# Performance work log

Measured on AMD Instinct MI355X. Metric: run time of the kernel, lower is better.

Reference implementation:

```python
import jax, jax.numpy as jnp
import numpy as np
import math

BLOCK = 4      # block_size
N_HEADS = 8
DIM = 512
COND = 512
B = 2
HWU = 32       # h = w = u
NN = 7         # 'cross' neighbors


def _layernorm(x, w, eps=1e-5):
    mu = x.mean(-1, keepdims=True)
    var = ((x - mu) ** 2).mean(-1, keepdims=True)
    return (x - mu) * jax.lax.rsqrt(var + eps) * w


def _modulate(x, shift, scale):
    return x * (1.0 + scale) + shift


def _rotate_half(x):
    x1, x2 = jnp.split(x, 2, axis=-1)
    return jnp.concatenate([-x2, x1], axis=-1)


def _rot(x, cos, sin):
    return x * cos + _rotate_half(x) * sin


def setup_inputs() -> dict:
    key = jax.random.key(0)
    ks = jax.random.split(key, 16)
    h = w = u = HWU
    S = h * w * u
    dh = DIM // N_HEADS
    P = BLOCK ** 3
    ib = HWU // BLOCK                       # blocks per axis = 8
    nb = ib ** 3                            # 512 blocks per batch

    x = jax.random.normal(ks[0], (B, S, DIM), jnp.float32)
    c = jax.random.normal(ks[1], (B, COND), jnp.float32)

    # proper rotary tables over P block-local positions
    inv = 1.0 / (10000.0 ** (np.arange(0, dh, 2, dtype=np.float32) / dh))
    f = np.arange(P, dtype=np.float32)[:, None] * inv[None, :]
    emb = np.concatenate([f, f], axis=-1)          # [P, dh]
    cos = jnp.asarray(np.cos(emb))[None, :, None, :]
    sin = jnp.asarray(np.sin(emb))[None, :, None, :]

    # neighbor indices (cross pattern) on the block grid, mirroring get_neighbor_indices
    grid = np.stack(np.meshgrid(np.arange(B), np.arange(ib), np.arange(ib), np.arange(ib), indexing='ij'), axis=-1)
    shifts = np.array([[0, 0, 0, 0], [0, 0, -1, 0], [0, -1, 0, 0], [0, 0, 0, -1],
                       [0, 0, 1, 0], [0, 1, 0, 0], [0, 0, 0, 1]])
    nbr = grid[..., None, :] + shifts[None, None, None, None, :, :]
    nbr[..., 1:] = np.clip(nbr[..., 1:], 0, ib - 1)
    flat = (nbr[..., 0] * ib * ib * ib + nbr[..., 1] * ib * ib
            + nbr[..., 2] * ib + nbr[..., 3]).reshape(B * nb, NN)
    # every other block is 'nonzero' -> Nsel = 512
    nonzero_blocks = np.arange(0, B * nb, 2, dtype=np.int64)
    nonzero_blocks_neighbor = flat[nonzero_blocks].reshape(-1).astype(np.int64)

    s = 0.02
    params = dict(
        norm1_w=jnp.ones((DIM,), jnp.float32),
        qkv_w=s * jax.random.normal(ks[2], (3 * DIM, DIM), jnp.float32),
        out_w=s * jax.random.normal(ks[3], (DIM, DIM), jnp.float32),
        norm2_w=jnp.ones((DIM,), jnp.float32),
        mlp_w1=s * jax.random.normal(ks[4], (4 * DIM, DIM), jnp.float32),
        mlp_b1=jnp.zeros((4 * DIM,), jnp.float32),
        mlp_w2=s * jax.random.normal(ks[5], (DIM, 4 * DIM), jnp.float32),
        mlp_b2=jnp.zeros((DIM,), jnp.float32),
        adaln_w=s * jax.random.normal(ks[6], (6 * DIM, COND), jnp.float32),
        adaln_b=jnp.zeros((6 * DIM,), jnp.float32),
        kv_empty=s * jax.random.normal(ks[7], (1, P, 2 * DIM), jnp.float32),
    )
    return dict(x=x, c=c, cos_q=cos, sin_q=sin, cos_k=cos, sin_k=sin,
                nonzero_blocks=jnp.asarray(nonzero_blocks),
                nonzero_blocks_neighbor=jnp.asarray(nonzero_blocks_neighbor),
                h=h, w=w, u=u, **params)


def reference(x, c, cos_q, sin_q, cos_k, sin_k, nonzero_blocks, nonzero_blocks_neighbor,
              h, w, u, norm1_w, qkv_w, out_w, norm2_w, mlp_w1, mlp_b1, mlp_w2, mlp_b2,
              adaln_w, adaln_b, kv_empty):
    Bx, S, D = x.shape
    bs = BLOCK
    ix, iy, iz = h // bs, w // bs, u // bs
    nb = ix * iy * iz
    P = bs ** 3
    dh = D // N_HEADS
    Nsel = nonzero_blocks.shape[0]

    def transform(t):
        t = t.reshape(Bx, ix, bs, iy, bs, iz, bs, D)
        return t.transpose(0, 1, 3, 5, 2, 4, 6, 7).reshape(Bx, nb, P, D)

    def inverse_transform(t):
        t = t.reshape(Bx, ix, iy, iz, bs, bs, bs, D)
        return t.transpose(0, 1, 4, 2, 5, 3, 6, 7).reshape(Bx, S, D)

    mods = (c @ adaln_w.T + adaln_b)[:, None, :]         # [B,1,6D]
    shift_msa, scale_msa, gate_msa, shift_mlp, scale_mlp, gate_mlp = jnp.split(mods, 6, axis=-1)

    x_skip = x
    xm = _modulate(_layernorm(x, norm1_w), shift_msa, scale_msa)
    xb = transform(xm).reshape(Bx * nb, P, D)
    x_sel = xb[nonzero_blocks]                            # [Nsel,P,D]

    qkv = x_sel @ qkv_w.T                                 # [Nsel,P,3D]
    q, k, v = jnp.split(qkv, 3, axis=-1)
    k_e, v_e = jnp.split(kv_empty, 2, axis=-1)            # [1,P,D]
    k_full = jnp.broadcast_to(k_e, (Bx * nb, P, D)).at[nonzero_blocks].set(k)
    v_full = jnp.broadcast_to(v_e, (Bx * nb, P, D)).at[nonzero_blocks].set(v)
    kn = k_full[nonzero_blocks_neighbor]                  # [Nsel*NN,P,D]
    vn = v_full[nonzero_blocks_neighbor]

    qh = _rot(q.reshape(Nsel, P, N_HEADS, dh), cos_q, sin_q)
    kh = _rot(kn.reshape(Nsel * NN, P, N_HEADS, dh), cos_k, sin_k)
    kh = kh.reshape(Nsel, NN * P, N_HEADS, dh)
    vh = vn.reshape(Nsel, NN * P, N_HEADS, dh)

    scores = jnp.einsum('bqhd,bkhd->bhqk', qh, kh) / math.sqrt(dh)
    attn = jax.nn.softmax(scores, axis=-1)
    out = jnp.einsum('bhqk,bkhd->bqhd', attn, vh).reshape(Nsel, P, D)

    xz = jnp.zeros((Bx * nb, P, D), out.dtype).at[nonzero_blocks].set(out)
    x_attn = inverse_transform(xz.reshape(Bx, nb, P, D))
    x1 = x_skip + gate_msa * (x_attn @ out_w.T)

    x2 = _modulate(_layernorm(x1, norm2_w), shift_mlp, scale_mlp)
    mlp = jax.nn.gelu(x2 @ mlp_w1.T + mlp_b1, approximate=True) @ mlp_w2.T + mlp_b2
    return x1 + gate_mlp * mlp
```

## Files before the change

kernel.cpp:

```cpp
#include <hip/hip_runtime.h>
#include <cstdint>
#include <cstddef>

typedef unsigned short u16;
typedef __attribute__((ext_vector_type(8))) __bf16 bf16x8;
typedef __attribute__((ext_vector_type(4))) float f32x4;

typedef __attribute__((address_space(1))) const void GAS;
typedef __attribute__((address_space(3))) void LAS;

__device__ __forceinline__ void gld_lds16(const void* g, void* l) {
  __builtin_amdgcn_global_load_lds((GAS*)g, (LAS*)l, 16, 0, 0);
}

__device__ __forceinline__ u16 f2bf(float f) {
  union { float f; unsigned u; } x; x.f = f;
  unsigned r = x.u + 0x7FFFu + ((x.u >> 16) & 1u);
  return (u16)(r >> 16);
}
__device__ __forceinline__ float bf2f(u16 s) {
  union { unsigned u; float f; } x; x.u = ((unsigned)s) << 16;
  return x.f;
}
__device__ __forceinline__ f32x4 mfma16(bf16x8 a, bf16x8 b, f32x4 c) {
  return __builtin_amdgcn_mfma_f32_16x16x32_bf16(a, b, c, 0, 0, 0);
}


__global__ void selmap_k(const int* __restrict__ nzb, int* __restrict__ map) {
  int t = threadIdx.x;
  map[t] = -1;
  __syncthreads();
  if (t < 512) map[nzb[t]] = t;
}

__global__ __launch_bounds__(256) void castw_k(const float* __restrict__ in,
                                               u16* __restrict__ out, int n4) {
  int i = blockIdx.x * 256 + threadIdx.x;
  if (i >= n4) return;
  float4 v = ((const float4*)in)[i];
  u16 o[4] = {f2bf(v.x), f2bf(v.y), f2bf(v.z), f2bf(v.w)};
  ((uint2*)out)[i] = *(uint2*)o;
}

__global__ __launch_bounds__(256) void adaln_k(const float* __restrict__ c,
    const float* __restrict__ w, const float* __restrict__ b, float* __restrict__ mods) {
  int j = blockIdx.x * 256 + threadIdx.x;
  int bt = blockIdx.y;
  const float4* cr = (const float4*)(c + bt * 512);
  const float4* wr = (const float4*)(w + (size_t)j * 512);
  float s = 0.f;
  #pragma unroll 4
  for (int k = 0; k < 128; ++k) {
    float4 a = wr[k], q = cr[k];
    s += a.x * q.x + a.y * q.y + a.z * q.z + a.w * q.w;
  }
  mods[bt * 3072 + j] = s + b[j];
}

__global__ __launch_bounds__(256) void kvempty_k(const float* __restrict__ kve,
    const float* __restrict__ cT, const float* __restrict__ sT,
    u16* __restrict__ kempty, u16* __restrict__ vTempty) {
  int T = blockIdx.x * 256 + threadIdx.x;
  int h = T >> 12, p = (T >> 6) & 63, d = T & 63;
  float kv = kve[p * 1024 + h * 64 + d];
  float pv = kve[p * 1024 + h * 64 + (d ^ 32)];
  float cs = cT[p * 64 + d], sn = sT[p * 64 + d];
  float r = kv * cs + ((d < 32) ? -pv : pv) * sn;
  kempty[(h * 64 + p) * 64 + d] = f2bf(r);
  vTempty[(h * 64 + d) * 64 + p] = f2bf(kve[p * 1024 + 512 + h * 64 + d]);
}


__global__ __launch_bounds__(256) void ln1_k(const float* __restrict__ x,
    const float* __restrict__ nw, const float* __restrict__ mods,
    const int* __restrict__ nzb, u16* __restrict__ xm) {
  int row = blockIdx.x * 4 + (threadIdx.x >> 6);
  int t = threadIdx.x & 63;
  int sel = row >> 6, p = row & 63;
  int g = nzb[sel];
  int bt = g >> 9, blk = g & 511;
  int s = (blk >> 6) * 4096 + (p >> 4) * 1024 + ((blk >> 3) & 7) * 128
        + ((p >> 2) & 3) * 32 + (blk & 7) * 4 + (p & 3);
  const float* src = x + ((size_t)bt * 32768 + s) * 512;
  int d0 = t * 8;
  float4 a = *(const float4*)(src + d0);
  float4 b = *(const float4*)(src + d0 + 4);
  float v[8] = {a.x, a.y, a.z, a.w, b.x, b.y, b.z, b.w};
  float sum = 0.f, sq = 0.f;
  #pragma unroll
  for (int j = 0; j < 8; ++j) { sum += v[j]; sq += v[j] * v[j]; }
  #pragma unroll
  for (int m = 1; m < 64; m <<= 1) {
    sum += __shfl_xor(sum, m, 64);
    sq  += __shfl_xor(sq, m, 64);
  }
  float mean = sum * (1.f / 512.f);
  float var = sq * (1.f / 512.f) - mean * mean;
  float rstd = rsqrtf(var + 1e-5f);
  const float* mb = mods + bt * 3072;
  u16 o[8];
  #pragma unroll
  for (int j = 0; j < 8; ++j) {
    int d = d0 + j;
    float xn = (v[j] - mean) * rstd * nw[d];
    o[j] = f2bf(xn * (1.f + mb[512 + d]) + mb[d]);
  }
  *(uint4*)(xm + (size_t)row * 512 + d0) = *(uint4*)o;
}


template <int EPI>
__global__ __launch_bounds__(512, 2) void gemm256(const u16* __restrict__ A,
    const u16* __restrict__ W, int M, int N, int K, void* __restrict__ outp,
    const float* __restrict__ bias, const u16* __restrict__ x1,
    const float* __restrict__ mods, int rowOff, int NB) {
  __shared__ u16 L[65536];
  const int nwg = gridDim.x;
  const int cpx = nwg >> 3;
  const int tile = ((int)blockIdx.x & 7) * cpx + ((int)blockIdx.x >> 3);
  const int bm = (tile / NB) * 256, bn = (tile % NB) * 256;
  const int tid = threadIdx.x;
  const int w = tid >> 6, l = tid & 63, lr = l & 15, lg = l >> 4;
  const int wr = w >> 2, wc = w & 3;

  const u16* ga[4];
  const u16* gb[4];
  #pragma unroll
  for (int i = 0; i < 4; ++i) {
    int s = i * 512 + tid;
    int r = s >> 3, c = (s & 7) ^ (r & 7);
    ga[i] = A + (size_t)(bm + r) * K + c * 8;
    gb[i] = W + (size_t)(bn + r) * K + c * 8;
  }

  f32x4 acc[8][4];
  #pragma unroll
  for (int i = 0; i < 8; ++i)
    #pragma unroll
    for (int j = 0; j < 4; ++j) acc[i][j] = (f32x4){0.f, 0.f, 0.f, 0.f};

  auto STAGE = [&](int kt, int buf) {
    u16* lb = L + buf * 32768;
    #pragma unroll
    for (int i = 0; i < 4; ++i) {
      gld_lds16(ga[i] + (size_t)kt * 64, lb + (i * 512 + tid) * 8);
      gld_lds16(gb[i] + (size_t)kt * 64, lb + 16384 + (i * 512 + tid) * 8);
    }
  };

  auto COMPUTE = [&](int buf) {
    const u16* LA = L + buf * 32768;
    const u16* LB = LA + 16384;
    bf16x8 bf[4][2];
    #pragma unroll
    for (int nf = 0; nf < 4; ++nf) {
      int Rb = wc * 64 + nf * 16 + lr;
      const u16* pb = LB + Rb * 64;
      int sw = Rb & 7;
      bf[nf][0] = *(const bf16x8*)(pb + ((lg ^ sw) << 3));
      bf[nf][1] = *(const bf16x8*)(pb + (((lg + 4) ^ sw) << 3));
    }
    __builtin_amdgcn_s_setprio(1);
    #pragma unroll
    for (int mf = 0; mf < 8; ++mf) {
      int Ra = wr * 128 + mf * 16 + lr;
      const u16* pa = LA + Ra * 64;
      int sw = Ra & 7;
      bf16x8 a0 = *(const bf16x8*)(pa + ((lg ^ sw) << 3));
      bf16x8 a1 = *(const bf16x8*)(pa + (((lg + 4) ^ sw) << 3));
      #pragma unroll
      for (int nf = 0; nf < 4; ++nf) {
        acc[mf][nf] = mfma16(a0, bf[nf][0], acc[mf][nf]);
        acc[mf][nf] = mfma16(a1, bf[nf][1], acc[mf][nf]);
      }
    }
    __builtin_amdgcn_s_setprio(0);
  };

  const int NT = K >> 6;
  STAGE(0, 0);
  for (int t = 0; t < NT - 1; ++t) {
    STAGE(t + 1, (t + 1) & 1);
    asm volatile("s_waitcnt vmcnt(8)" ::: "memory");
    __builtin_amdgcn_s_barrier();
    asm volatile("" ::: "memory");
    COMPUTE(t & 1);
    asm volatile("" ::: "memory");
    __builtin_amdgcn_s_barrier();
  }
  asm volatile("s_waitcnt vmcnt(0)" ::: "memory");
  __builtin_amdgcn_s_barrier();
  asm volatile("" ::: "memory");
  COMPUTE((NT - 1) & 1);

  const int row0 = bm + wr * 128, col0 = bn + wc * 64;
  #pragma unroll
  for (int mf = 0; mf < 8; ++mf) {
    #pragma unroll
    for (int nf = 0; nf < 4; ++nf) {
      #pragma unroll
      for (int j = 0; j < 4; ++j) {
        int row = row0 + mf * 16 + lg * 4 + j;
        int col = col0 + nf * 16 + lr;
        float v = acc[mf][nf][j];
        if constexpr (EPI == 0) {
          ((u16*)outp)[(size_t)row * N + col] = f2bf(v);
        } else if constexpr (EPI == 1) {
          ((float*)outp)[(size_t)row * N + col] = v;
        } else if constexpr (EPI == 2) {
          v += bias[col];
          float z = 1.5957691216057308f * (v + 0.044715f * v * v * v);
          float t = 1.f - 2.f / (1.f + __expf(z));
          ((u16*)outp)[(size_t)row * N + col] = f2bf(0.5f * v * (1.f + t));
        } else {
          v += bias[col];
          int grow = rowOff + row;
          int bt = grow >> 15;
          float gate = mods[bt * 3072 + 2560 + col];
          ((float*)outp)[(size_t)grow * 512 + col] =
              bf2f(x1[(size_t)grow * 512 + col]) + gate * v;
        }
      }
    }
  }
}


__global__ __launch_bounds__(256) void ropepack_k(const u16* __restrict__ qkv,
    const float* __restrict__ cq, const float* __restrict__ sq,
    const float* __restrict__ ck, const float* __restrict__ sk,
    u16* __restrict__ qb, u16* __restrict__ kb) {
  int T = blockIdx.x * 256 + threadIdx.x;
  int row = T >> 7, oct = T & 127;
  int c0 = oct * 8;
  int sel = row >> 6, p = row & 63;
  int isk = (c0 >= 512);
  int chn = c0 & 511;
  int h = chn >> 6, d0 = chn & 63;
  int lower = (d0 < 32);
  const u16* base = qkv + (size_t)row * 1536 + (isk ? 512 : 0) + h * 64;
  u16 vm[8], vp[8];
  *(uint4*)vm = *(const uint4*)(base + d0);
  *(uint4*)vp = *(const uint4*)(base + (d0 ^ 32));
  const float* cT = (isk ? ck : cq) + p * 64 + d0;
  const float* sT = (isk ? sk : sq) + p * 64 + d0;
  float scale = isk ? 1.f : 0.125f;
  u16 o[8];
  #pragma unroll
  for (int j = 0; j < 8; ++j) {
    float a = bf2f(vm[j]), b = bf2f(vp[j]);
    float r = a * cT[j] + (lower ? -b : b) * sT[j];
    o[j] = f2bf(r * scale);
  }
  u16* dst = (isk ? kb : qb) + (((size_t)sel * 8 + h) * 64 + p) * 64 + d0;
  *(uint4*)dst = *(uint4*)o;
}


__global__ __launch_bounds__(256) void vtrans_k(const u16* __restrict__ qkv,
                                                u16* __restrict__ vT) {
  __shared__ u16 tb[64 * 65];
  int sel = blockIdx.x >> 3, h = blockIdx.x & 7;
  int tid = threadIdx.x;
  int p = tid >> 2, q16 = (tid & 3) * 16;
  const u16* src = qkv + (size_t)(sel * 64 + p) * 1536 + 1024 + h * 64 + q16;
  u16 ld[16];
  *(uint4*)&ld[0] = *(const uint4*)src;
  *(uint4*)&ld[8] = *(const uint4*)(src + 8);
  #pragma unroll
  for (int j = 0; j < 16; ++j) tb[p * 65 + q16 + j] = ld[j];
  __syncthreads();
  int d = tid >> 2, po = (tid & 3) * 16;
  u16 o[16];
  #pragma unroll
  for (int j = 0; j < 16; ++j) o[j] = tb[(po + j) * 65 + d];
  u16* dst = vT + (((size_t)sel * 8 + h) * 64 + d) * 64 + po;
  *(uint4*)dst = *(uint4*)&o[0];
  *(uint4*)(dst + 8) = *(uint4*)&o[8];
}


__global__ __launch_bounds__(256, 4) void attn_k(const u16* __restrict__ qbuf,
    const u16* __restrict__ kfull, const u16* __restrict__ vT,
    const u16* __restrict__ kempty, const u16* __restrict__ vTempty,
    const int* __restrict__ nbrs, const int* __restrict__ selmap,
    u16* __restrict__ attnout) {
  __shared__ u16 KB[2][4096];
  __shared__ u16 Pl[4][16][72];
  int bid = blockIdx.x;
  int swz = (bid & 7) * 512 + (bid >> 3);
  int sel = swz >> 3, h = swz & 7;
  int tid = threadIdx.x;
  int w = tid >> 6, l = tid & 63, lr = l & 15, lg = l >> 4;

  int mmv[7];
  #pragma unroll
  for (int n = 0; n < 7; ++n) mmv[n] = selmap[nbrs[sel * 7 + n]];

  const u16* qg = qbuf + (((size_t)sel * 8 + h) * 64 + w * 16) * 64;
  bf16x8 qf0 = *(const bf16x8*)(qg + lr * 64 + lg * 8);
  bf16x8 qf1 = *(const bf16x8*)(qg + lr * 64 + 32 + lg * 8);

  int srow = tid >> 3;
  int soff = srow * 64 + (((tid & 7) ^ (srow & 7)) << 3);
  size_t hoff = (size_t)h * 4096;

  {
    const u16* kp = (mmv[0] >= 0) ? kfull + (size_t)mmv[0] * 32768 + hoff
                                  : kempty + hoff;
    gld_lds16(kp + soff, &KB[0][w * 512]);
    gld_lds16(kp + soff + 2048, &KB[0][2048 + w * 512]);
  }

  f32x4 o[4];
  float mrun[4], lrun[4];
  #pragma unroll
  for (int ct = 0; ct < 4; ++ct) o[ct] = (f32x4){0.f, 0.f, 0.f, 0.f};
  #pragma unroll
  for (int r = 0; r < 4; ++r) { mrun[r] = -1e30f; lrun[r] = 0.f; }

  #pragma unroll
  for (int n = 0; n < 7; ++n) {
    if (n < 6) {
      const u16* kp = (mmv[n + 1] >= 0) ? kfull + (size_t)mmv[n + 1] * 32768 + hoff
                                        : kempty + hoff;
      int b = (n + 1) & 1;
      gld_lds16(kp + soff, &KB[b][w * 512]);
      gld_lds16(kp + soff + 2048, &KB[b][2048 + w * 512]);
      asm volatile("s_waitcnt vmcnt(2)" ::: "memory");
    } else {
      asm volatile("s_waitcnt vmcnt(0)" ::: "memory");
    }
    __builtin_amdgcn_s_barrier();
    __builtin_amdgcn_sched_barrier(0);

    const u16* kl = &KB[n & 1][0];
    const u16* vp = (mmv[n] >= 0) ? vT + (size_t)mmv[n] * 32768 + hoff
                                  : vTempty + hoff;
    f32x4 s4[4];
    int xr = lr & 7;
    #pragma unroll
    for (int ct = 0; ct < 4; ++ct) {
      int row = ct * 16 + lr;
      bf16x8 b0 = *(const bf16x8*)(kl + row * 64 + ((lg ^ xr) << 3));
      bf16x8 b1 = *(const bf16x8*)(kl + row * 64 + (((lg + 4) ^ xr) << 3));
      f32x4 z = (f32x4){0.f, 0.f, 0.f, 0.f};
      z = mfma16(qf0, b0, z);
      z = mfma16(qf1, b1, z);
      s4[ct] = z;
    }
    float rmax[4], sc[4], rs[4];
    #pragma unroll
    for (int r = 0; r < 4; ++r)
      rmax[r] = fmaxf(fmaxf(s4[0][r], s4[1][r]), fmaxf(s4[2][r], s4[3][r]));
    #pragma unroll
    for (int r = 0; r < 4; ++r) {
      #pragma unroll
      for (int ms = 1; ms < 16; ms <<= 1)
        rmax[r] = fmaxf(rmax[r], __shfl_xor(rmax[r], ms, 64));
      float mn = fmaxf(mrun[r], rmax[r]);
      sc[r] = __expf(mrun[r] - mn);
      mrun[r] = mn;
      rs[r] = 0.f;
    }
    #pragma unroll
    for (int ct = 0; ct < 4; ++ct)
      #pragma unroll
      for (int r = 0; r < 4; ++r) {
        float e = __expf(s4[ct][r] - mrun[r]);
        s4[ct][r] = e;
        rs[r] += e;
      }
    #pragma unroll
    for (int r = 0; r < 4; ++r) {
      #pragma unroll
      for (int ms = 1; ms < 16; ms <<= 1) rs[r] += __shfl_xor(rs[r], ms, 64);
      lrun[r] = lrun[r] * sc[r] + rs[r];
    }
    #pragma unroll
    for (int ct = 0; ct < 4; ++ct)
      #pragma unroll
      for (int r = 0; r < 4; ++r) o[ct][r] *= sc[r];
    #pragma unroll
    for (int ct = 0; ct < 4; ++ct)
      #pragma unroll
      for (int r = 0; r < 4; ++r)
        Pl[w][lg * 4 + r][ct * 16 + lr] = f2bf(s4[ct][r]);
    asm volatile("s_waitcnt lgkmcnt(0)" ::: "memory");
    __builtin_amdgcn_sched_barrier(0);
    bf16x8 pa0 = *(const bf16x8*)&Pl[w][lr][lg * 8];
    bf16x8 pa1 = *(const bf16x8*)&Pl[w][lr][32 + lg * 8];
    #pragma unroll
    for (int ct = 0; ct < 4; ++ct) {
      bf16x8 v0 = *(const bf16x8*)(vp + (ct * 16 + lr) * 64 + lg * 8);
      bf16x8 v1 = *(const bf16x8*)(vp + (ct * 16 + lr) * 64 + 32 + lg * 8);
      o[ct] = mfma16(pa0, v0, o[ct]);
      o[ct] = mfma16(pa1, v1, o[ct]);
    }
    asm volatile("" ::: "memory");
    __builtin_amdgcn_s_barrier();
    __builtin_amdgcn_sched_barrier(0);
  }

  float inv[4];
  #pragma unroll
  for (int r = 0; r < 4; ++r) inv[r] = 1.f / lrun[r];
  #pragma unroll
  for (int ct = 0; ct < 4; ++ct)
    #pragma unroll
    for (int r = 0; r < 4; ++r) {
      int p = w * 16 + lg * 4 + r;
      int d = ct * 16 + lr;
      attnout[((size_t)sel * 64 + p) * 512 + h * 64 + d] = f2bf(o[ct][r] * inv[r]);
    }
}


__global__ __launch_bounds__(256) void x1ln2_k(const float* __restrict__ x,
    const float* __restrict__ opout, const int* __restrict__ selmap,
    const float* __restrict__ mods, const float* __restrict__ nw,
    u16* __restrict__ x1, u16* __restrict__ x2) {
  int row = blockIdx.x * 4 + (threadIdx.x >> 6);
  int t = threadIdx.x & 63;
  int bt = row >> 15, s = row & 32767;
  int i1 = s >> 12, p1 = (s >> 10) & 3, i2 = (s >> 7) & 7,
      p2 = (s >> 5) & 3, i3 = (s >> 2) & 7, p3 = s & 3;
  int blk = (((i1 << 3) | i2) << 3) | i3;
  int m = selmap[(bt << 9) | blk];
  int d0 = t * 8;
  const float* src = x + (size_t)row * 512 + d0;
  float4 a = *(const float4*)src;
  float4 b = *(const float4*)(src + 4);
  float v[8] = {a.x, a.y, a.z, a.w, b.x, b.y, b.z, b.w};
  const float* mb = mods + bt * 3072;
  if (m >= 0) {
    int p = (p1 << 4) | (p2 << 2) | p3;
    const float* op = opout + ((size_t)m * 64 + p) * 512 + d0;
    float4 oa = *(const float4*)op;
    float4 ob = *(const float4*)(op + 4);
    float ov[8] = {oa.x, oa.y, oa.z, oa.w, ob.x, ob.y, ob.z, ob.w};
    #pragma unroll
    for (int j = 0; j < 8; ++j) v[j] += mb[1024 + d0 + j] * ov[j];
  }
  u16 o1[8];
  #pragma unroll
  for (int j = 0; j < 8; ++j) o1[j] = f2bf(v[j]);
  *(uint4*)(x1 + (size_t)row * 512 + d0) = *(uint4*)o1;
  float sum = 0.f, sq = 0.f;
  #pragma unroll
  for (int j = 0; j < 8; ++j) { sum += v[j]; sq += v[j] * v[j]; }
  #pragma unroll
  for (int mm = 1; mm < 64; mm <<= 1) {
    sum += __shfl_xor(sum, mm, 64);
    sq  += __shfl_xor(sq, mm, 64);
  }
  float mean = sum * (1.f / 512.f);
  float var = sq * (1.f / 512.f) - mean * mean;
  float rstd = rsqrtf(var + 1e-5f);
  u16 o[8];
  #pragma unroll
  for (int j = 0; j < 8; ++j) {
    int d = d0 + j;
    float xn = (v[j] - mean) * rstd * nw[d];
    o[j] = f2bf(xn * (1.f + mb[2048 + d]) + mb[1536 + d]);
  }
  *(uint4*)(x2 + (size_t)row * 512 + d0) = *(uint4*)o;
}


extern "C" void kernel_launch(void* const* d_in, const int* in_sizes, int n_in,
                              void* d_out, int out_size, void* d_ws, size_t ws_size,
                              hipStream_t stream) {
  const float* x    = (const float*)d_in[0];
  const float* c    = (const float*)d_in[1];
  const float* cosq = (const float*)d_in[2];
  const float* sinq = (const float*)d_in[3];
  const float* cosk = (const float*)d_in[4];
  const float* sink = (const float*)d_in[5];
  const int* nzb    = (const int*)d_in[6];
  const int* nbrs   = (const int*)d_in[7];
  const float* norm1_w = (const float*)d_in[11];
  const float* qkv_w   = (const float*)d_in[12];
  const float* out_w   = (const float*)d_in[13];
  const float* norm2_w = (const float*)d_in[14];
  const float* mlp_w1  = (const float*)d_in[15];
  const float* mlp_b1  = (const float*)d_in[16];
  const float* mlp_w2  = (const float*)d_in[17];
  const float* mlp_b2  = (const float*)d_in[18];
  const float* adaln_w = (const float*)d_in[19];
  const float* adaln_b = (const float*)d_in[20];
  const float* kv_e    = (const float*)d_in[21];
  float* outp = (float*)d_out;
  char* ws = (char*)d_ws;

  const size_t MB = 1024ull * 1024ull;
  u16*   qkvb    = (u16*)(ws + 0);
  float* opout   = (float*)(ws + 0);
  u16*   hidden  = (u16*)(ws + 0);
  u16*   xm      = (u16*)(ws + 96 * MB);
  u16*   attnout = (u16*)(ws + 96 * MB);
  u16*   qb      = (u16*)(ws + 128 * MB);
  u16*   kf      = (u16*)(ws + 160 * MB);
  u16*   vT      = (u16*)(ws + 192 * MB);
  u16*   x1      = (u16*)(ws + 256 * MB);
  u16*   x2      = (u16*)(ws + 320 * MB);
  char*  S0      = ws + 384 * MB;
  float* mods    = (float*)(S0);
  int*   selmap  = (int*)(S0 + 0x8000);
  u16*   kempty  = (u16*)(S0 + 0x10000);
  u16*   vTempty = (u16*)(S0 + 0x20000);
  u16*   qkvw_bf = (u16*)(S0 + 0x30000);
  u16*   outw_bf = qkvw_bf + (size_t)1536 * 512;
  u16*   w1_bf   = outw_bf + (size_t)512 * 512;
  u16*   w2_bf   = w1_bf + (size_t)2048 * 512;

  selmap_k<<<1, 1024, 0, stream>>>(nzb, selmap);
  adaln_k<<<dim3(12, 2), 256, 0, stream>>>(c, adaln_w, adaln_b, mods);
  castw_k<<<768, 256, 0, stream>>>(qkv_w, qkvw_bf, 1536 * 512 / 4);
  castw_k<<<256, 256, 0, stream>>>(out_w, outw_bf, 512 * 512 / 4);
  castw_k<<<1024, 256, 0, stream>>>(mlp_w1, w1_bf, 2048 * 512 / 4);
  castw_k<<<1024, 256, 0, stream>>>(mlp_w2, w2_bf, 512 * 2048 / 4);
  kvempty_k<<<128, 256, 0, stream>>>(kv_e, cosk, sink, kempty, vTempty);

  ln1_k<<<8192, 256, 0, stream>>>(x, norm1_w, mods, nzb, xm);

  gemm256<0><<<768, 512, 0, stream>>>(xm, qkvw_bf, 32768, 1536, 512, qkvb,
                                      nullptr, nullptr, nullptr, 0, 6);
  ropepack_k<<<16384, 256, 0, stream>>>(qkvb, cosq, sinq, cosk, sink, qb, kf);
  vtrans_k<<<4096, 256, 0, stream>>>(qkvb, vT);

  attn_k<<<4096, 256, 0, stream>>>(qb, kf, vT, kempty, vTempty, nbrs, selmap, attnout);

  gemm256<1><<<256, 512, 0, stream>>>(attnout, outw_bf, 32768, 512, 512, opout,
                                      nullptr, nullptr, nullptr, 0, 2);

  x1ln2_k<<<16384, 256, 0, stream>>>(x, opout, selmap, mods, norm2_w, x1, x2);

  gemm256<2><<<2048, 512, 0, stream>>>(x2, w1_bf, 65536, 2048, 512, hidden,
                                       mlp_b1, nullptr, nullptr, 0, 8);
  gemm256<3><<<512, 512, 0, stream>>>(hidden, w2_bf, 65536, 512, 2048, outp,
                                      mlp_b2, x1, mods, 0, 2);
}
```

Measured before the change: 946.6 us.

## Switch GEMMs to 128x128 tiles, fuse RoPE into QKV GEMM, simplify attention K loads

Replaces the 256x256/K64 GEMM with a 128x128/K32 tile kernel at 256 threads and higher occupancy. Rotary embedding and Q/K packing move into the QKV GEMM epilogue, and V is written to a compact buffer, which removes the separate ropepack pass. The output-projection result is stored as bf16 instead of fp32, and the attention kernel reads K straight from global memory instead of double-buffering it through LDS. Smaller tiles cut per-block reuse and add launch and traffic overhead. The unstaged K reads and bf16 rounding may also cost speed and accuracy.

After: 973.3 us. 1.03x slower.

```diff
diff --git a/kernel.cpp b/kernel.cpp
--- a/kernel.cpp
+++ b/kernel.cpp
@@ -111,92 +111,84 @@
 
 
 template <int EPI>
-__global__ __launch_bounds__(512, 2) void gemm256(const u16* __restrict__ A,
+__global__ __launch_bounds__(256, 4) void gemm128(const u16* __restrict__ A,
     const u16* __restrict__ W, int M, int N, int K, void* __restrict__ outp,
     const float* __restrict__ bias, const u16* __restrict__ x1,
-    const float* __restrict__ mods, int rowOff, int NB) {
-  __shared__ u16 L[65536];
+    const float* __restrict__ mods, int NB,
+    const float* __restrict__ cq, const float* __restrict__ sq,
+    const float* __restrict__ ck, const float* __restrict__ sk,
+    u16* __restrict__ qb, u16* __restrict__ kb, u16* __restrict__ vb) {
+  __shared__ u16 L[2][8192];
   const int nwg = gridDim.x;
   const int cpx = nwg >> 3;
   const int tile = ((int)blockIdx.x & 7) * cpx + ((int)blockIdx.x >> 3);
-  const int bm = (tile / NB) * 256, bn = (tile % NB) * 256;
+  const int bm = (tile / NB) * 128, bn = (tile % NB) * 128;
   const int tid = threadIdx.x;
   const int w = tid >> 6, l = tid & 63, lr = l & 15, lg = l >> 4;
-  const int wr = w >> 2, wc = w & 3;
-
-  const u16* ga[4];
-  const u16* gb[4];
-  #pragma unroll
-  for (int i = 0; i < 4; ++i) {
-    int s = i * 512 + tid;
-    int r = s >> 3, c = (s & 7) ^ (r & 7);
-    ga[i] = A + (size_t)(bm + r) * K + c * 8;
-    gb[i] = W + (size_t)(bn + r) * K + c * 8;
-  }
-
-  f32x4 acc[8][4];
-  #pragma unroll
-  for (int i = 0; i < 8; ++i)
+  const int wr = w >> 1, wc = w & 1;
+
+  const int s0 = tid, s1 = 256 + tid;
+  const int rA0 = s0 >> 2, j0 = (s0 & 3) ^ ((s0 >> 3) & 3);
+  const int rA1 = s1 >> 2, j1 = (s1 & 3) ^ ((s1 >> 3) & 3);
+  const u16* gA0 = A + (size_t)(bm + rA0) * K + j0 * 8;
+  const u16* gA1 = A + (size_t)(bm + rA1) * K + j1 * 8;
+  const u16* gB0 = W + (size_t)(bn + rA0) * K + j0 * 8;
+  const u16* gB1 = W + (size_t)(bn + rA1) * K + j1 * 8;
+
+  f32x4 acc[4][4];
+  #pragma unroll
+  for (int i = 0; i < 4; ++i)
     #pragma unroll
     for (int j = 0; j < 4; ++j) acc[i][j] = (f32x4){0.f, 0.f, 0.f, 0.f};
 
   auto STAGE = [&](int kt, int buf) {
-    u16* lb = L + buf * 32768;
-    #pragma unroll
-    for (int i = 0; i < 4; ++i) {
-      gld_lds16(ga[i] + (size_t)kt * 64, lb + (i * 512 + tid) * 8);
-      gld_lds16(gb[i] + (size_t)kt * 64, lb + 16384 + (i * 512 + tid) * 8);
-    }
+    u16* lb = &L[buf][0];
+    gld_lds16(gA0 + (size_t)kt * 32, lb + s0 * 8);
+    gld_lds16(gA1 + (size_t)kt * 32, lb + s1 * 8);
+    gld_lds16(gB0 + (size_t)kt * 32, lb + 4096 + s0 * 8);
+    gld_lds16(gB1 + (size_t)kt * 32, lb + 4096 + s1 * 8);
   };
-
   auto COMPUTE = [&](int buf) {
-    const u16* LA = L + buf * 32768;
-    const u16* LB = LA + 16384;
-    bf16x8 bf[4][2];
+    const u16* base = &L[buf][0];
+    bf16x8 bfr[4];
     #pragma unroll
     for (int nf = 0; nf < 4; ++nf) {
-      int Rb = wc * 64 + nf * 16 + lr;
-      const u16* pb = LB + Rb * 64;
-      int sw = Rb & 7;
-      bf[nf][0] = *(const bf16x8*)(pb + ((lg ^ sw) << 3));
-      bf[nf][1] = *(const bf16x8*)(pb + (((lg + 4) ^ sw) << 3));
+      int rB = wc * 64 + nf * 16 + lr;
+      bfr[nf] = *(const bf16x8*)(base + 4096 + rB * 32 + ((lg ^ ((rB >> 1) & 3)) << 3));
     }
     __builtin_amdgcn_s_setprio(1);
     #pragma unroll
-    for (int mf = 0; mf < 8; ++mf) {
-      int Ra = wr * 128 + mf * 16 + lr;
-      const u16* pa = LA + Ra * 64;
-      int sw = Ra & 7;
-      bf16x8 a0 = *(const bf16x8*)(pa + ((lg ^ sw) << 3));
-      bf16x8 a1 = *(const bf16x8*)(pa + (((lg + 4) ^ sw) << 3));
-      #pragma unroll
-      for (int nf = 0; nf < 4; ++nf) {
-        acc[mf][nf] = mfma16(a0, bf[nf][0], acc[mf][nf]);
-        acc[mf][nf] = mfma16(a1, bf[nf][1], acc[mf][nf]);
-      }
+    for (int mf = 0; mf < 4; ++mf) {
+      int rA = wr * 64 + mf * 16 + lr;
+      bf16x8 a = *(const bf16x8*)(base + rA * 32 + ((lg ^ ((rA >> 1) & 3)) << 3));
+      #pragma unroll
+      for (int nf = 0; nf < 4; ++nf)
+        acc[mf][nf] = mfma16(a, bfr[nf], acc[mf][nf]);
     }
     __builtin_amdgcn_s_setprio(0);
   };
 
-  const int NT = K >> 6;
+  const int NT = K >> 5;
   STAGE(0, 0);
-  for (int t = 0; t < NT - 1; ++t) {
-    STAGE(t + 1, (t + 1) & 1);
-    asm volatile("s_waitcnt vmcnt(8)" ::: "memory");
+  for (int t = 0; t < NT; ++t) {
+    if (t + 1 < NT) {
+      STAGE(t + 1, (t + 1) & 1);
+      asm volatile("s_waitcnt vmcnt(4)" ::: "memory");
+    } else {
+      asm volatile("s_waitcnt vmcnt(0)" ::: "memory");
+    }
+    __builtin_amdgcn_sched_barrier(0);
     __builtin_amdgcn_s_barrier();
     asm volatile("" ::: "memory");
     COMPUTE(t & 1);
     asm volatile("" ::: "memory");
     __builtin_amdgcn_s_barrier();
-  }
-  asm volatile("s_waitcnt vmcnt(0)" ::: "memory");
-  __builtin_amdgcn_s_barrier();
-  asm volatile("" ::: "memory");
-  COMPUTE((NT - 1) & 1);
-
-  const int row0 = bm + wr * 128, col0 = bn + wc * 64;
-  #pragma unroll
-  for (int mf = 0; mf < 8; ++mf) {
+    __builtin_amdgcn_sched_barrier(0);
+  }
+
+  const int row0 = bm + wr * 64, col0 = bn + wc * 64;
+  #pragma unroll
+  for (int mf = 0; mf < 4; ++mf) {
     #pragma unroll
     for (int nf = 0; nf < 4; ++nf) {
       #pragma unroll
@@ -206,20 +198,33 @@
         float v = acc[mf][nf][j];
         if constexpr (EPI == 0) {
           ((u16*)outp)[(size_t)row * N + col] = f2bf(v);
-        } else if constexpr (EPI == 1) {
-          ((float*)outp)[(size_t)row * N + col] = v;
         } else if constexpr (EPI == 2) {
           v += bias[col];
           float z = 1.5957691216057308f * (v + 0.044715f * v * v * v);
           float t = 1.f - 2.f / (1.f + __expf(z));
           ((u16*)outp)[(size_t)row * N + col] = f2bf(0.5f * v * (1.f + t));
+        } else if constexpr (EPI == 3) {
+          v += bias[col];
+          int bt = row >> 15;
+          float gate = mods[bt * 3072 + 2560 + col];
+          ((float*)outp)[(size_t)row * 512 + col] =
+              bf2f(x1[(size_t)row * 512 + col]) + gate * v;
         } else {
-          v += bias[col];
-          int grow = rowOff + row;
-          int bt = grow >> 15;
-          float gate = mods[bt * 3072 + 2560 + col];
-          ((float*)outp)[(size_t)grow * 512 + col] =
-              bf2f(x1[(size_t)grow * 512 + col]) + gate * v;
+          int sel = row >> 6, p = row & 63;
+          if (col < 1024) {
+            int isk = col >= 512;
+            int h = (col >> 6) & 7, d64 = col & 63;
+            int lower = (d64 < 32);
+            float pv = acc[mf][nf ^ 2][j];
+            const float* cT = isk ? ck : cq;
+            const float* sT = isk ? sk : sq;
+            float r = v * cT[p * 64 + d64] + (lower ? -pv : pv) * sT[p * 64 + d64];
+            if (!isk) r *= 0.125f;
+            u16* dst = (isk ? kb : qb) + (((size_t)sel * 8 + h) * 64 + p) * 64 + d64;
+            *dst = f2bf(r);
+          } else {
+            vb[(size_t)row * 512 + (col - 1024)] = f2bf(v);
+          }
         }
       }
     }
@@ -227,44 +232,13 @@
 }
 
 
-__global__ __launch_bounds__(256) void ropepack_k(const u16* __restrict__ qkv,
-    const float* __restrict__ cq, const float* __restrict__ sq,
-    const float* __restrict__ ck, const float* __restrict__ sk,
-    u16* __restrict__ qb, u16* __restrict__ kb) {
-  int T = blockIdx.x * 256 + threadIdx.x;
-  int row = T >> 7, oct = T & 127;
-  int c0 = oct * 8;
-  int sel = row >> 6, p = row & 63;
-  int isk = (c0 >= 512);
-  int chn = c0 & 511;
-  int h = chn >> 6, d0 = chn & 63;
-  int lower = (d0 < 32);
-  const u16* base = qkv + (size_t)row * 1536 + (isk ? 512 : 0) + h * 64;
-  u16 vm[8], vp[8];
-  *(uint4*)vm = *(const uint4*)(base + d0);
-  *(uint4*)vp = *(const uint4*)(base + (d0 ^ 32));
-  const float* cT = (isk ? ck : cq) + p * 64 + d0;
-  const float* sT = (isk ? sk : sq) + p * 64 + d0;
-  float scale = isk ? 1.f : 0.125f;
-  u16 o[8];
-  #pragma unroll
-  for (int j = 0; j < 8; ++j) {
-    float a = bf2f(vm[j]), b = bf2f(vp[j]);
-    float r = a * cT[j] + (lower ? -b : b) * sT[j];
-    o[j] = f2bf(r * scale);
-  }
-  u16* dst = (isk ? kb : qb) + (((size_t)sel * 8 + h) * 64 + p) * 64 + d0;
-  *(uint4*)dst = *(uint4*)o;
-}
-
-
-__global__ __launch_bounds__(256) void vtrans_k(const u16* __restrict__ qkv,
+__global__ __launch_bounds__(256) void vtrans_k(const u16* __restrict__ vbuf,
                                                 u16* __restrict__ vT) {
   __shared__ u16 tb[64 * 65];
   int sel = blockIdx.x >> 3, h = blockIdx.x & 7;
   int tid = threadIdx.x;
   int p = tid >> 2, q16 = (tid & 3) * 16;
-  const u16* src = qkv + (size_t)(sel * 64 + p) * 1536 + 1024 + h * 64 + q16;
+  const u16* src = vbuf + (size_t)(sel * 64 + p) * 512 + h * 64 + q16;
   u16 ld[16];
   *(uint4*)&ld[0] = *(const uint4*)src;
   *(uint4*)&ld[8] = *(const uint4*)(src + 8);
@@ -286,7 +260,6 @@
     const u16* __restrict__ kempty, const u16* __restrict__ vTempty,
     const int* __restrict__ nbrs, const int* __restrict__ selmap,
     u16* __restrict__ attnout) {
-  __shared__ u16 KB[2][4096];
   __shared__ u16 Pl[4][16][72];
   int bid = blockIdx.x;
   int swz = (bid & 7) * 512 + (bid >> 3);
@@ -301,17 +274,7 @@
   const u16* qg = qbuf + (((size_t)sel * 8 + h) * 64 + w * 16) * 64;
   bf16x8 qf0 = *(const bf16x8*)(qg + lr * 64 + lg * 8);
   bf16x8 qf1 = *(const bf16x8*)(qg + lr * 64 + 32 + lg * 8);
-
-  int srow = tid >> 3;
-  int soff = srow * 64 + (((tid & 7) ^ (srow & 7)) << 3);
   size_t hoff = (size_t)h * 4096;
-
-  {
-    const u16* kp = (mmv[0] >= 0) ? kfull + (size_t)mmv[0] * 32768 + hoff
-                                  : kempty + hoff;
-    gld_lds16(kp + soff, &KB[0][w * 512]);
-    gld_lds16(kp + soff + 2048, &KB[0][2048 + w * 512]);
-  }
 
   f32x4 o[4];
   float mrun[4], lrun[4];
@@ -322,29 +285,15 @@
 
   #pragma unroll
   for (int n = 0; n < 7; ++n) {
-    if (n < 6) {
-      const u16* kp = (mmv[n + 1] >= 0) ? kfull + (size_t)mmv[n + 1] * 32768 + hoff
-                                        : kempty + hoff;
-      int b = (n + 1) & 1;
-      gld_lds16(kp + soff, &KB[b][w * 512]);
-      gld_lds16(kp + soff + 2048, &KB[b][2048 + w * 512]);
-      asm volatile("s_waitcnt vmcnt(2)" ::: "memory");
-    } else {
-      asm volatile("s_waitcnt vmcnt(0)" ::: "memory");
-    }
-    __builtin_amdgcn_s_barrier();
-    __builtin_amdgcn_sched_barrier(0);
-
-    const u16* kl = &KB[n & 1][0];
+    const u16* kp = (mmv[n] >= 0) ? kfull + (size_t)mmv[n] * 32768 + hoff
+                                  : kempty + hoff;
     const u16* vp = (mmv[n] >= 0) ? vT + (size_t)mmv[n] * 32768 + hoff
                                   : vTempty + hoff;
     f32x4 s4[4];
-    int xr = lr & 7;
     #pragma unroll
     for (int ct = 0; ct < 4; ++ct) {
-      int row = ct * 16 + lr;
-      bf16x8 b0 = *(const bf16x8*)(kl + row * 64 + ((lg ^ xr) << 3));
-      bf16x8 b1 = *(const bf16x8*)(kl + row * 64 + (((lg + 4) ^ xr) << 3));
+      bf16x8 b0 = *(const bf16x8*)(kp + (ct * 16 + lr) * 64 + lg * 8);
+      bf16x8 b1 = *(const bf16x8*)(kp + (ct * 16 + lr) * 64 + 32 + lg * 8);
       f32x4 z = (f32x4){0.f, 0.f, 0.f, 0.f};
       z = mfma16(qf0, b0, z);
       z = mfma16(qf1, b1, z);
@@ -398,8 +347,6 @@
       o[ct] = mfma16(pa0, v0, o[ct]);
       o[ct] = mfma16(pa1, v1, o[ct]);
     }
-    asm volatile("" ::: "memory");
-    __builtin_amdgcn_s_barrier();
     __builtin_amdgcn_sched_barrier(0);
   }
 
@@ -418,7 +365,7 @@
 
 
 __global__ __launch_bounds__(256) void x1ln2_k(const float* __restrict__ x,
-    const float* __restrict__ opout, const int* __restrict__ selmap,
+    const u16* __restrict__ opout, const int* __restrict__ selmap,
     const float* __restrict__ mods, const float* __restrict__ nw,
     u16* __restrict__ x1, u16* __restrict__ x2) {
   int row = blockIdx.x * 4 + (threadIdx.x >> 6);
@@ -436,12 +383,11 @@
   const float* mb = mods + bt * 3072;
   if (m >= 0) {
     int p = (p1 << 4) | (p2 << 2) | p3;
-    const float* op = opout + ((size_t)m * 64 + p) * 512 + d0;
-    float4 oa = *(const float4*)op;
-    float4 ob = *(const float4*)(op + 4);
-    float ov[8] = {oa.x, oa.y, oa.z, oa.w, ob.x, ob.y, ob.z, ob.w};
-    #pragma unroll
-    for (int j = 0; j < 8; ++j) v[j] += mb[1024 + d0 + j] * ov[j];
+    const u16* op = opout + ((size_t)m * 64 + p) * 512 + d0;
+    u16 oh[8];
+    *(uint4*)oh = *(const uint4*)op;
+    #pragma unroll
+    for (int j = 0; j < 8; ++j) v[j] += mb[1024 + d0 + j] * bf2f(oh[j]);
   }
   u16 o1[8];
   #pragma unroll
@@ -495,8 +441,8 @@
   char* ws = (char*)d_ws;
 
   const size_t MB = 1024ull * 1024ull;
-  u16*   qkvb    = (u16*)(ws + 0);
-  float* opout   = (float*)(ws + 0);
+  u16*   vbuf    = (u16*)(ws + 0);
+  u16*   opout   = (u16*)(ws + 0);
   u16*   hidden  = (u16*)(ws + 0);
   u16*   xm      = (u16*)(ws + 96 * MB);
   u16*   attnout = (u16*)(ws + 96 * MB);
@@ -525,20 +471,26 @@
 
   ln1_k<<<8192, 256, 0, stream>>>(x, norm1_w, mods, nzb, xm);
 
-  gemm256<0><<<768, 512, 0, stream>>>(xm, qkvw_bf, 32768, 1536, 512, qkvb,
-                                      nullptr, nullptr, nullptr, 0, 6);
-  ropepack_k<<<16384, 256, 0, stream>>>(qkvb, cosq, sinq, cosk, sink, qb, kf);
-  vtrans_k<<<4096, 256, 0, stream>>>(qkvb, vT);
+  gemm128<4><<<3072, 256, 0, stream>>>(xm, qkvw_bf, 32768, 1536, 512, nullptr,
+                                       nullptr, nullptr, nullptr, 12,
+                                       cosq, sinq, cosk, sink, qb, kf, vbuf);
+  vtrans_k<<<4096, 256, 0, stream>>>(vbuf, vT);
 
   attn_k<<<4096, 256, 0, stream>>>(qb, kf, vT, kempty, vTempty, nbrs, selmap, attnout);
 
-  gemm256<1><<<256, 512, 0, stream>>>(attnout, outw_bf, 32768, 512, 512, opout,
-                                      nullptr, nullptr, nullptr, 0, 2);
+  gemm128<0><<<1024, 256, 0, stream>>>(attnout, outw_bf, 32768, 512, 512, opout,
+                                       nullptr, nullptr, nullptr, 4,
+                                       nullptr, nullptr, nullptr, nullptr,
+                                       nullptr, nullptr, nullptr);
 
   x1ln2_k<<<16384, 256, 0, stream>>>(x, opout, selmap, mods, norm2_w, x1, x2);
 
-  gemm256<2><<<2048, 512, 0, stream>>>(x2, w1_bf, 65536, 2048, 512, hidden,
-                                       mlp_b1, nullptr, nullptr, 0, 8);
-  gemm256<3><<<512, 512, 0, stream>>>(hidden, w2_bf, 65536, 512, 2048, outp,
-                                      mlp_b2, x1, mods, 0, 2);
-}
+  gemm128<2><<<8192, 256, 0, stream>>>(x2, w1_bf, 65536, 2048, 512, hidden,
+                                       mlp_b1, nullptr, nullptr, 16,
+                                       nullptr, nullptr, nullptr, nullptr,
+                                       nullptr, nullptr, nullptr);
+  gemm128<3><<<2048, 256, 0, stream>>>(hidden, w2_bf, 65536, 512, 2048, outp,
+                                       mlp_b2, x1, mods, 4,
+                                       nullptr, nullptr, nullptr, nullptr,
+                                       nullptr, nullptr, nullptr);
+}
```
